# Performance work log

Measured on AMD Instinct MI355X. Metric: run time of the kernel, lower is better.

Reference implementation:

```python
import jax, jax.numpy as jnp
import numpy as np


def _rgcn_layer(h, Wr, Ws, src, dst, rel, norm):
    # h: [N,d], Wr: [R,d,d] per-relation weight, Ws: [d,d] self-loop weight
    N, d = h.shape
    R = Wr.shape[0]
    E = src.shape[0]
    msg = jnp.zeros((E, d), h.dtype)
    for r in range(R):  # R is small/static; transform-then-gather per relation
        hW = h @ Wr[r]              # [N,d]
        msg = jnp.where((rel == r)[:, None], hW[src], msg)  # [E,d]
    agg = jax.ops.segment_sum(msg * norm[:, None], dst, num_segments=N)
    return jax.nn.relu(agg + h @ Ws)


def _calc_score(emb, w_relation, es, er, eo):
    # DistMult-style bilinear score: s^T W_r o per target edge
    s = emb[es]                     # [T,d]
    o = emb[eo]                     # [T,d]
    R = w_relation.shape[0]
    sW = jnp.zeros_like(s)
    for r in range(R):
        sW = jnp.where((er == r)[:, None], s @ w_relation[r], sW)
    return jnp.sum(sW * o, axis=-1)  # [T]


def setup_inputs() -> dict:
    key = jax.random.key(0)
    ks = jax.random.split(key, 16)
    N, E, T, d, R, L = 20000, 160000, 50000, 768, 8, 2
    sc = 1.0 / np.sqrt(d)
    return {
        "node_feat": jax.random.normal(ks[0], (N, d), jnp.float32),
        "edge_norm": jax.random.uniform(ks[1], (E,), jnp.float32),
        "W_rel": jax.random.normal(ks[2], (L, R, d, d), jnp.float32) * sc,
        "W_self": jax.random.normal(ks[3], (L, d, d), jnp.float32) * sc,
        "w_relation": jax.random.normal(ks[4], (R, d, d), jnp.float32) * sc,
        "src": jax.random.randint(ks[5], (E,), 0, N, jnp.int32),
        "dst": jax.random.randint(ks[6], (E,), 0, N, jnp.int32),
        "rel": jax.random.randint(ks[7], (E,), 0, R, jnp.int32),
        "pos_src": jax.random.randint(ks[8], (T,), 0, N, jnp.int32),
        "pos_rel": jax.random.randint(ks[9], (T,), 0, R, jnp.int32),
        "pos_dst": jax.random.randint(ks[10], (T,), 0, N, jnp.int32),
        "neg_src": jax.random.randint(ks[11], (T,), 0, N, jnp.int32),
        "neg_rel": jax.random.randint(ks[12], (T,), 0, R, jnp.int32),
        "neg_dst": jax.random.randint(ks[13], (T,), 0, N, jnp.int32),
    }


def reference(node_feat, edge_norm, W_rel, W_self, w_relation,
              src, dst, rel, pos_src, pos_rel, pos_dst,
              neg_src, neg_rel, neg_dst):
    h = node_feat
    L = W_rel.shape[0]
    for l in range(L):
        h = _rgcn_layer(h, W_rel[l], W_self[l], src, dst, rel, edge_norm)
    es = jnp.concatenate([pos_src, neg_src])
    er = jnp.concatenate([pos_rel, neg_rel])
    eo = jnp.concatenate([pos_dst, neg_dst])
    score = _calc_score(h, w_relation, es, er, eo)  # [2T]
    return score
```

## Files before the change

### kernel.cpp

```cpp
#include <hip/hip_runtime.h>

typedef float f32x4 __attribute__((ext_vector_type(4)));
typedef __bf16 bf16x8 __attribute__((ext_vector_type(8)));
typedef unsigned short u16x8 __attribute__((ext_vector_type(8)));
typedef unsigned short u16x4 __attribute__((ext_vector_type(4)));

static __device__ __forceinline__ unsigned short f2bf(float f) {
  unsigned int x = __builtin_bit_cast(unsigned int, f);
  x += 0x7FFFu + ((x >> 16) & 1u);
  return (unsigned short)(x >> 16);
}
static __device__ __forceinline__ float bf2f(unsigned short h) {
  unsigned int x = ((unsigned int)h) << 16;
  return __builtin_bit_cast(float, x);
}

static __device__ __forceinline__ void gload_lds16(const unsigned short* g,
                                                   unsigned short* l) {
  __builtin_amdgcn_global_load_lds(
      (const __attribute__((address_space(1))) void*)g,
      (__attribute__((address_space(3))) void*)l, 16, 0, 0);
}

__global__ __launch_bounds__(256) void k_f32_to_bf16(
    const float* __restrict__ in, unsigned short* __restrict__ out, int n4) {
  int i = blockIdx.x * 256 + threadIdx.x;
  if (i >= n4) return;
  float4 v = reinterpret_cast<const float4*>(in)[i];
  u16x4 o = {f2bf(v.x), f2bf(v.y), f2bf(v.z), f2bf(v.w)};
  reinterpret_cast<u16x4*>(out)[i] = o;
}

__global__ __launch_bounds__(256) void k_transpose_w(
    const float* __restrict__ in, unsigned short* __restrict__ out,
    int G, int SL, int j0) {
  __shared__ float tile[32][33];
  const int D = 768;
  int z = blockIdx.z;
  int j = j0 + z % G, grp = z / G;
  const float* A = in + (size_t)z * D * D;
  const size_t ld = (size_t)SL * D;
  unsigned short* O = out + (size_t)grp * D * ld + (size_t)j * D;
  int nt = blockIdx.x * 32, kt = blockIdx.y * 32;
  int tx = threadIdx.x, ty = threadIdx.y;
#pragma unroll
  for (int i = 0; i < 4; ++i)
    tile[ty + i * 8][tx] = A[(size_t)(kt + ty + i * 8) * D + nt + tx];
  __syncthreads();
#pragma unroll
  for (int i = 0; i < 4; ++i)
    O[(size_t)(nt + ty + i * 8) * ld + kt + tx] = f2bf(tile[tx][ty + i * 8]);
}

__global__ __launch_bounds__(256) void k_hist(const int* __restrict__ dst,
                                              const int* __restrict__ rel,
                                              int* __restrict__ cnt, int E, int NV) {
  int e = blockIdx.x * 256 + threadIdx.x;
  if (e < E) atomicAdd(&cnt[rel[e] * NV + dst[e]], 1);
}

__global__ __launch_bounds__(256) void k_hist_t(
    const int* __restrict__ ps, const int* __restrict__ pr,
    const int* __restrict__ ns, const int* __restrict__ nr,
    int* __restrict__ cnt, int T, int NV) {
  int t = blockIdx.x * 256 + threadIdx.x;
  if (t >= 2 * T) return;
  int s = (t < T) ? ps[t] : ns[t - T];
  int r = (t < T) ? pr[t] : nr[t - T];
  atomicAdd(&cnt[r * NV + s], 1);
}

__global__ __launch_bounds__(256) void k_part(const int* __restrict__ cnt,
                                              int* __restrict__ bsum, int n) {
  __shared__ int wsums[4];
  int blk = blockIdx.x, tid = threadIdx.x;
  int base = blk * 1024 + tid * 4;
  int s = 0;
#pragma unroll
  for (int j = 0; j < 4; ++j) {
    int i = base + j;
    if (i < n) s += cnt[i];
  }
#pragma unroll
  for (int d = 1; d < 64; d <<= 1) s += __shfl_xor(s, d, 64);
  if ((tid & 63) == 0) wsums[tid >> 6] = s;
  __syncthreads();
  if (tid == 0) bsum[blk] = wsums[0] + wsums[1] + wsums[2] + wsums[3];
}

__global__ __launch_bounds__(1024) void k_scan_b(const int* __restrict__ bsum,
                                                 int* __restrict__ bscan, int nb,
                                                 int* __restrict__ off_total) {
  __shared__ int wpre[16];
  int tid = threadIdx.x, lane = tid & 63, w = tid >> 6;
  int v = (tid < nb) ? bsum[tid] : 0;
  int inc = v;
#pragma unroll
  for (int d = 1; d < 64; d <<= 1) {
    int t = __shfl_up(inc, d, 64);
    if (lane >= d) inc += t;
  }
  if (lane == 63) wpre[w] = inc;
  __syncthreads();
  if (w == 0) {
    int vv = (lane < 16) ? wpre[lane] : 0;
    int p = vv;
#pragma unroll
    for (int d = 1; d < 16; d <<= 1) {
      int t = __shfl_up(p, d, 64);
      if (lane >= d) p += t;
    }
    if (lane < 16) wpre[lane] = p - vv;
  }
  __syncthreads();
  if (tid < nb) bscan[tid] = wpre[w] + inc - v;
  if (tid == 1023) *off_total = wpre[15] + inc;
}

__global__ __launch_bounds__(256) void k_scan_f(const int* __restrict__ cnt,
                                                const int* __restrict__ bscan,
                                                int* __restrict__ off, int n) {
  __shared__ int wpre[4];
  int blk = blockIdx.x, tid = threadIdx.x, lane = tid & 63, w = tid >> 6;
  int base = blk * 1024 + tid * 4;
  int v[4];
  int s = 0;
#pragma unroll
  for (int j = 0; j < 4; ++j) {
    int i = base + j;
    v[j] = (i < n) ? cnt[i] : 0;
    s += v[j];
  }
  int inc = s;
#pragma unroll
  for (int d = 1; d < 64; d <<= 1) {
    int t = __shfl_up(inc, d, 64);
    if (lane >= d) inc += t;
  }
  if (lane == 63) wpre[w] = inc;
  __syncthreads();
  int wb = 0;
  for (int j = 0; j < w; ++j) wb += wpre[j];
  int run = bscan[blk] + wb + (inc - s);
#pragma unroll
  for (int j = 0; j < 4; ++j) {
    int i = base + j;
    if (i < n) off[i] = run;
    run += v[j];
  }
}

__global__ __launch_bounds__(256) void k_bucket(
    const int* __restrict__ src, const int* __restrict__ dst,
    const int* __restrict__ rel, const float* __restrict__ norm,
    const int* __restrict__ off, int* __restrict__ fill,
    int* __restrict__ spack, float* __restrict__ snorm, int E, int NV) {
  int e = blockIdx.x * 256 + threadIdx.x;
  if (e >= E) return;
  int key = rel[e] * NV + dst[e];
  int slot = off[key] + atomicAdd(&fill[key], 1);
  spack[slot] = src[e];
  snorm[slot] = norm[e];
}

__global__ __launch_bounds__(512) void k_tprep(
    const int* __restrict__ off2, int* __restrict__ tpo, int* __restrict__ rbase,
    int* __restrict__ btile, int NV, int R, int TB) {
  __shared__ int tpo_s[17];
  int tid = threadIdx.x;
  if (tid == 0) {
    int run = 0;
    for (int r = 0; r < R; ++r) {
      rbase[r] = off2[r * NV];
      int tot = off2[(r + 1) * NV] - off2[r * NV];
      tpo_s[r] = run;
      run += (tot + 255) & ~255;
    }
    tpo_s[R] = run;
    for (int r = 0; r <= R; ++r) tpo[r] = tpo_s[r];
  }
  __syncthreads();
  for (int mt = tid; mt < TB; mt += 512) {
    int base = mt * 256;
    int b = -1;
    if (base < tpo_s[R]) {
      for (int r = 0; r < R; ++r)
        if (base >= tpo_s[r] && base < tpo_s[r + 1]) { b = r; break; }
    }
    btile[mt] = b;
  }
}

__global__ __launch_bounds__(256) void k_tbucket3(
    const int* __restrict__ ps, const int* __restrict__ pr, const int* __restrict__ pd,
    const int* __restrict__ ns, const int* __restrict__ nr, const int* __restrict__ nd,
    const int* __restrict__ off2, int* __restrict__ fill,
    const int* __restrict__ tpo, const int* __restrict__ rbase,
    int* __restrict__ sidx, int* __restrict__ oidx, int* __restrict__ tmap,
    int T, int NV) {
  int t = blockIdx.x * 256 + threadIdx.x;
  if (t >= 2 * T) return;
  int s, r, o;
  if (t < T) { s = ps[t]; r = pr[t]; o = pd[t]; }
  else       { s = ns[t - T]; r = nr[t - T]; o = nd[t - T]; }
  int key = r * NV + s;
  int rank = atomicAdd(&fill[key], 1);
  int slot = tpo[r] + (off2[key] - rbase[r]) + rank;
  sidx[slot] = s;
  oidx[slot] = o;
  tmap[slot] = t;
}

__global__ __launch_bounds__(256) void k_gather(
    const unsigned short* __restrict__ h, const int* __restrict__ off,
    const int* __restrict__ spack, const float* __restrict__ snorm,
    unsigned short* __restrict__ Acat, int NV, int r0, int r1, int ld) {
  int v = (blockIdx.x * 256 + threadIdx.x) >> 6;
  int lane = threadIdx.x & 63;
  int col = lane * 4;
  for (int r = r0; r < r1; ++r) {
    float a[12];
#pragma unroll
    for (int j = 0; j < 12; ++j) a[j] = 0.f;
    if (v < NV) {
      int beg = off[r * NV + v], end = off[r * NV + v + 1];
      for (int p = beg; p < end; ++p) {
        const unsigned short* row = h + (size_t)spack[p] * 768 + col;
        float nm = snorm[p];
#pragma unroll
        for (int c = 0; c < 3; ++c) {
          u16x4 vv = *reinterpret_cast<const u16x4*>(row + c * 256);
#pragma unroll
          for (int j = 0; j < 4; ++j) a[c * 4 + j] += nm * bf2f(vv[j]);
        }
      }
    }
    unsigned short* orow = Acat + (size_t)v * ld + (size_t)(r - r0) * 768 + col;
#pragma unroll
    for (int c = 0; c < 3; ++c) {
      u16x4 o = {f2bf(a[c * 4 + 0]), f2bf(a[c * 4 + 1]),
                 f2bf(a[c * 4 + 2]), f2bf(a[c * 4 + 3])};
      *reinterpret_cast<u16x4*>(orow + c * 256) = o;
    }
  }
}

#define STAGE_A(BUF, HALF, TT)                                                   \
  do {                                                                           \
    const unsigned short* _s =                                                   \
        A + (size_t)(m0 + (HALF) * 128 + srow) * K + (size_t)(TT) * 64 + gcol;   \
    gload_lds16(_s, &As[BUF][HALF][w << 3][0]);                                  \
    gload_lds16(_s + (size_t)64 * K, &As[BUF][HALF][64 + (w << 3)][0]);          \
  } while (0)
#define STAGE_B(BUF, HALF, TT)                                                   \
  do {                                                                           \
    const unsigned short* _s =                                                   \
        B + (size_t)(n0 + (HALF) * 128 + srow) * K + (size_t)(TT) * 64 + gcol;   \
    gload_lds16(_s, &Bs[BUF][HALF][w << 3][0]);                                  \
    gload_lds16(_s + (size_t)64 * K, &Bs[BUF][HALF][64 + (w << 3)][0]);          \
  } while (0)
#define GEMM_PRE()                                                               \
  const int tid = threadIdx.x;                                                   \
  const int lane = tid & 63;                                                     \
  const int w = tid >> 6;                                                        \
  const int wr = w >> 2;                                                         \
  const int wc = w & 3;                                                          \
  const int lr = lane & 15, lg = lane >> 4;                                      \
  int bid = blockIdx.x;                                                          \
  const int per = 8 * NT;                                                        \
  int grp = bid / per, rem = bid % per;                                          \
  int mstart = grp * 8;                                                          \
  int gsz = MT - mstart;                                                         \
  if (gsz > 8) gsz = 8;                                                          \
  const int mt = mstart + rem % gsz;                                             \
  const int ntile = rem / gsz;                                                   \
  const int m0 = mt * 256, n0 = ntile * 256;                                     \
  const int srow = tid >> 3;                                                     \
  const int gcol = (((tid & 7) ^ (tid >> 3)) & 7) * 8;                           \
  const int nk = K >> 6;
#define R_BV6(BUF)                                                               \
  _Pragma("unroll") for (int nb = 0; nb < 2; ++nb)                               \
  _Pragma("unroll") for (int j = 0; j < 2; ++j)                                  \
  _Pragma("unroll") for (int kk = 0; kk < 2; ++kk)                               \
      bv[nb][j][kk] = *reinterpret_cast<const bf16x8*>(                          \
          &Bs[BUF][nb][wc * 32 + j * 16 + lr][((lg + 4 * kk) ^ (lr & 7)) * 8]);
#define R_AF6(BUF, HALF)                                                         \
  _Pragma("unroll") for (int i = 0; i < 4; ++i)                                  \
  _Pragma("unroll") for (int kk = 0; kk < 2; ++kk)                               \
      af[i][kk] = *reinterpret_cast<const bf16x8*>(                              \
          &As[BUF][HALF][wr * 64 + i * 16 + lr][((lg + 4 * kk) ^ (lr & 7)) * 8]);
#define GEMM_LOOP(STAGEA_MACRO)                                                  \
  bf16x8 af[4][2], bv[2][2][2];                                                  \
  for (int t = 0; t < nk; ++t) {                                                 \
    const int buf = t & 1;                                                       \
    if (t + 1 < nk)                                                              \
      asm volatile("s_waitcnt vmcnt(4)" ::: "memory");                           \
    else                                                                         \
      asm volatile("s_waitcnt vmcnt(0)" ::: "memory");                           \
    __builtin_amdgcn_s_barrier();                                                \
    asm volatile("" ::: "memory");                                               \
    R_AF6(buf, 0);                                                               \
    R_BV6(buf);                                                                  \
    if (t + 1 < nk) {                                                            \
      STAGEA_MACRO(buf ^ 1, 1, t + 1);                                           \
      STAGE_B(buf ^ 1, 0, t + 1);                                                \
    }                                                                            \
    __builtin_amdgcn_s_setprio(1);                                               \
    _Pragma("unroll") for (int i = 0; i < 4; ++i)                                \
    _Pragma("unroll") for (int nb = 0; nb < 2; ++nb)                             \
    _Pragma("unroll") for (int j = 0; j < 2; ++j)                                \
    _Pragma("unroll") for (int kk = 0; kk < 2; ++kk)                             \
        acc[0][nb][i][j] = __builtin_amdgcn_mfma_f32_16x16x32_bf16(              \
            af[i][kk], bv[nb][j][kk], acc[0][nb][i][j], 0, 0, 0);                \
    __builtin_amdgcn_s_setprio(0);                                               \
    asm volatile("" ::: "memory");                                               \
    __builtin_amdgcn_s_barrier();                                                \
    asm volatile("" ::: "memory");                                               \
    R_AF6(buf, 1);                                                               \
    if (t + 2 < nk) {                                                            \
      STAGEA_MACRO(buf, 0, t + 2);                                               \
      STAGE_B(buf, 1, t + 2);                                                    \
    }                                                                            \
    __builtin_amdgcn_s_setprio(1);                                               \
    _Pragma("unroll") for (int i = 0; i < 4; ++i)                                \
    _Pragma("unroll") for (int nb = 0; nb < 2; ++nb)                             \
    _Pragma("unroll") for (int j = 0; j < 2; ++j)                                \
    _Pragma("unroll") for (int kk = 0; kk < 2; ++kk)                             \
        acc[1][nb][i][j] = __builtin_amdgcn_mfma_f32_16x16x32_bf16(              \
            af[i][kk], bv[nb][j][kk], acc[1][nb][i][j], 0, 0, 0);                \
    __builtin_amdgcn_s_setprio(0);                                               \
  }

template <int EPI>
__global__ __launch_bounds__(512, 2) void k_gemm_tn(
    const unsigned short* __restrict__ A, const unsigned short* __restrict__ B,
    void* __restrict__ Cp, const float* __restrict__ C0,
    int M, int N, int K, int MT, int NT) {
  __shared__ unsigned short As[2][2][128][64];
  __shared__ unsigned short Bs[2][2][128][64];
  GEMM_PRE();
  f32x4 acc[2][2][4][2] = {};

  STAGE_A(0, 0, 0);
  STAGE_B(0, 1, 0);
  STAGE_A(0, 1, 0);
  STAGE_B(0, 0, 0);
  if (nk > 1) {
    STAGE_A(1, 0, 1);
    STAGE_B(1, 1, 1);
  }
  GEMM_LOOP(STAGE_A);

#pragma unroll
  for (int ma = 0; ma < 2; ++ma)
#pragma unroll
    for (int i = 0; i < 4; ++i)
#pragma unroll
      for (int q = 0; q < 4; ++q) {
        int r = m0 + ma * 128 + wr * 64 + i * 16 + lg * 4 + q;
        if (r >= M) continue;
#pragma unroll
        for (int nb = 0; nb < 2; ++nb)
#pragma unroll
          for (int j = 0; j < 2; ++j) {
            int cn = n0 + nb * 128 + wc * 32 + j * 16 + lr;
            float v = acc[ma][nb][i][j][q];
            size_t idx = (size_t)r * N + cn;
            if (EPI == 1) {
              v += C0[idx];
              v = v > 0.f ? v : 0.f;
              ((unsigned short*)Cp)[idx] = f2bf(v);
            } else {
              ((float*)Cp)[idx] = v + C0[idx];
            }
          }
      }
}

#define STAGE_AH(BUF, HALF, TT)                                                  \
  do {                                                                           \
    const unsigned short* _sa =                                                  \
        ((TT) < nkA) ? paA##HALF##a + (size_t)(TT) * 64                          \
                     : paH##HALF##a + (size_t)((TT)-nkA) * 64;                   \
    gload_lds16(_sa, &As[BUF][HALF][w << 3][0]);                                 \
    const unsigned short* _sb =                                                  \
        ((TT) < nkA) ? paA##HALF##b + (size_t)(TT) * 64                          \
                     : paH##HALF##b + (size_t)((TT)-nkA) * 64;                   \
    gload_lds16(_sb, &As[BUF][HALF][64 + (w << 3)][0]);                          \
  } while (0)

__global__ __launch_bounds__(512, 2) void k_gemm_fuse(
    const unsigned short* __restrict__ Ac, const unsigned short* __restrict__ hA,
    const unsigned short* __restrict__ B, float* __restrict__ Cp,
    int M, int N, int K, int KA, int MT, int NT) {
  __shared__ unsigned short As[2][2][128][64];
  __shared__ unsigned short Bs[2][2][128][64];
  GEMM_PRE();
  const int nkA = KA >> 6;
  const unsigned short* paA0a = Ac + (size_t)(m0 + srow) * KA + gcol;
  const unsigned short* paA0b = Ac + (size_t)(m0 + 64 + srow) * KA + gcol;
  const unsigned short* paA1a = Ac + (size_t)(m0 + 128 + srow) * KA + gcol;
  const unsigned short* paA1b = Ac + (size_t)(m0 + 192 + srow) * KA + gcol;
  const unsigned short* paH0a = hA + (size_t)(m0 + srow) * 768 + gcol;
  const unsigned short* paH0b = hA + (size_t)(m0 + 64 + srow) * 768 + gcol;
  const unsigned short* paH1a = hA + (size_t)(m0 + 128 + srow) * 768 + gcol;
  const unsigned short* paH1b = hA + (size_t)(m0 + 192 + srow) * 768 + gcol;

  f32x4 acc[2][2][4][2] = {};

  STAGE_AH(0, 0, 0);
  STAGE_B(0, 1, 0);
  STAGE_AH(0, 1, 0);
  STAGE_B(0, 0, 0);
  if (nk > 1) {
    STAGE_AH(1, 0, 1);
    STAGE_B(1, 1, 1);
  }
  GEMM_LOOP(STAGE_AH);

#pragma unroll
  for (int ma = 0; ma < 2; ++ma)
#pragma unroll
    for (int i = 0; i < 4; ++i)
#pragma unroll
      for (int q = 0; q < 4; ++q) {
        int r = m0 + ma * 128 + wr * 64 + i * 16 + lg * 4 + q;
        if (r >= M) continue;
#pragma unroll
        for (int nb = 0; nb < 2; ++nb)
#pragma unroll
          for (int j = 0; j < 2; ++j) {
            int cn = n0 + nb * 128 + wc * 32 + j * 16 + lr;
            Cp[(size_t)r * N + cn] = acc[ma][nb][i][j][q];
          }
      }
}

#define STAGE_AI(BUF, HALF, TT)                                                  \
  do {                                                                           \
    gload_lds16(pa##HALF##a + (size_t)(TT) * 64, &As[BUF][HALF][w << 3][0]);     \
    gload_lds16(pa##HALF##b + (size_t)(TT) * 64,                                 \
                &As[BUF][HALF][64 + (w << 3)][0]);                               \
  } while (0)

__global__ __launch_bounds__(512, 2) void k_gemm_score(
    const unsigned short* __restrict__ h, const unsigned short* __restrict__ Bw,
    float* __restrict__ out, const int* __restrict__ sidx,
    const int* __restrict__ oidx, const int* __restrict__ tmap,
    const int* __restrict__ btile, int MT, int NT) {
  const int K = 768;
  __shared__ unsigned short As[2][2][128][64];
  __shared__ unsigned short Bs[2][2][128][64];
  GEMM_PRE();
  const int bt = btile[mt];
  if (bt < 0) return;
  const unsigned short* B = Bw + (size_t)bt * K * K;
  const unsigned short* pa0a = h + (size_t)sidx[m0 + srow] * K + gcol;
  const unsigned short* pa0b = h + (size_t)sidx[m0 + 64 + srow] * K + gcol;
  const unsigned short* pa1a = h + (size_t)sidx[m0 + 128 + srow] * K + gcol;
  const unsigned short* pa1b = h + (size_t)sidx[m0 + 192 + srow] * K + gcol;

  f32x4 acc[2][2][4][2] = {};

  STAGE_AI(0, 0, 0);
  STAGE_B(0, 1, 0);
  STAGE_AI(0, 1, 0);
  STAGE_B(0, 0, 0);
  STAGE_AI(1, 0, 1);
  STAGE_B(1, 1, 1);
  GEMM_LOOP(STAGE_AI);

#pragma unroll
  for (int ma = 0; ma < 2; ++ma)
#pragma unroll
    for (int i = 0; i < 4; ++i)
#pragma unroll
      for (int q = 0; q < 4; ++q) {
        int slot = m0 + ma * 128 + wr * 64 + i * 16 + lg * 4 + q;
        int t = tmap[slot];
        float p = 0.f;
        if (t >= 0) {
          const unsigned short* orow = h + (size_t)oidx[slot] * K;
#pragma unroll
          for (int nb = 0; nb < 2; ++nb)
#pragma unroll
            for (int j = 0; j < 2; ++j) {
              int cn = n0 + nb * 128 + wc * 32 + j * 16 + lr;
              p += acc[ma][nb][i][j][q] * bf2f(orow[cn]);
            }
        }
#pragma unroll
        for (int d = 1; d < 16; d <<= 1) p += __shfl_xor(p, d, 64);
        if (t >= 0 && lr == 0) unsafeAtomicAdd(&out[t], p);
      }
}

extern "C" void kernel_launch(void* const* d_in, const int* in_sizes, int n_in,
                              void* d_out, int out_size, void* d_ws, size_t ws_size,
                              hipStream_t stream) {
  const float* node_feat = (const float*)d_in[0];
  const float* edge_norm = (const float*)d_in[1];
  const float* W_rel = (const float*)d_in[2];
  const float* W_self = (const float*)d_in[3];
  const float* w_relation = (const float*)d_in[4];
  const int* src = (const int*)d_in[5];
  const int* dst = (const int*)d_in[6];
  const int* rel = (const int*)d_in[7];
  const int* pos_src = (const int*)d_in[8];
  const int* pos_rel = (const int*)d_in[9];
  const int* pos_dst = (const int*)d_in[10];
  const int* neg_src = (const int*)d_in[11];
  const int* neg_rel = (const int*)d_in[12];
  const int* neg_dst = (const int*)d_in[13];

  const int D = 768;
  const int NV = in_sizes[0] / D;
  const int E = in_sizes[1];
  const int L = in_sizes[3] / (D * D);
  const int R = in_sizes[4] / (D * D);
  const int T = in_sizes[8];
  const int Mpad = (NV + 255) & ~255;
  const int RN = R * NV;
  const int NB = (RN + 1023) / 1024;
  const int TB = (2 * T + R * 256 + 255) / 256;
  const int Mbound = TB * 256;

  auto align_up = [](size_t x) { return (x + 255) & ~(size_t)255; };
  size_t sz_wt_rel = align_up((size_t)L * (R + 1) * D * D * 2);
  size_t sz_wt_score = align_up((size_t)R * D * D * 2);
  size_t sz_h = align_up((size_t)Mpad * D * 2);
  size_t sz_agg = align_up((size_t)Mpad * D * 4);
  size_t sz_cntfill = align_up((size_t)2 * RN * 4);
  size_t sz_off = align_up((size_t)(RN + 8) * 4);
  size_t sz_sp = align_up((size_t)E * 4);
  size_t sz_bs = align_up((size_t)2 * (NB + 8) * 4);
  size_t sz_tix = align_up((size_t)Mbound * 4);
  size_t sz_tsmall = align_up((size_t)(TB + 64) * 4);
  size_t fixed = sz_wt_rel + sz_wt_score + sz_h + sz_agg + sz_cntfill +
                 2 * sz_off + 2 * sz_sp + sz_bs + 3 * sz_tix + sz_tsmall;
  int RG = 4;
  while (RG > 1 && fixed + align_up((size_t)Mpad * RG * D * 2) > ws_size) RG >>= 1;
  const int NGRP = R / RG;
  const size_t LW = (size_t)(R + 1) * D * D;

  char* wp = (char*)d_ws;
  unsigned short* wt_rel = (unsigned short*)wp; wp += sz_wt_rel;
  unsigned short* wt_score = (unsigned short*)wp; wp += sz_wt_score;
  unsigned short* h = (unsigned short*)wp; wp += sz_h;
  float* agg = (float*)wp; wp += sz_agg;
  int* cnt = (int*)wp; int* fill = cnt + RN; wp += sz_cntfill;
  int* off = (int*)wp; wp += sz_off;
  int* off2 = (int*)wp; wp += sz_off;
  int* spack = (int*)wp; wp += sz_sp;
  float* snorm = (float*)wp; wp += sz_sp;
  int* bsum = (int*)wp; int* bscan = bsum + NB + 4; wp += sz_bs;
  int* sidx = (int*)wp; wp += sz_tix;
  int* oidx = (int*)wp; wp += sz_tix;
  int* tmap = (int*)wp; wp += sz_tix;
  int* btile = (int*)wp;
  int* tpo = btile + TB + 8;
  int* rbase = tpo + R + 2;
  wp += sz_tsmall;
  unsigned short* Acat = (unsigned short*)wp;

  dim3 tb32(32, 8);
  k_f32_to_bf16<<<(NV * D / 4 + 255) / 256, 256, 0, stream>>>(node_feat, h, NV * D / 4);
  if (Mpad > NV)
    hipMemsetAsync(h + (size_t)NV * D, 0, (size_t)(Mpad - NV) * D * 2, stream);
  for (int l = 0; l < L; ++l) {
    k_transpose_w<<<dim3(24, 24, RG), tb32, 0, stream>>>(
        W_rel + (size_t)l * R * D * D, wt_rel + (size_t)l * LW, RG, RG + 1, 0);
    k_transpose_w<<<dim3(24, 24, 1), tb32, 0, stream>>>(
        W_self + (size_t)l * D * D, wt_rel + (size_t)l * LW, 1, RG + 1, RG);
    for (int gi = 1; gi < NGRP; ++gi)
      k_transpose_w<<<dim3(24, 24, RG), tb32, 0, stream>>>(
          W_rel + (size_t)(l * R + gi * RG) * D * D,
          wt_rel + (size_t)l * LW + (size_t)(RG + 1) * D * D +
              (size_t)(gi - 1) * RG * D * D, RG, RG, 0);
  }
  k_transpose_w<<<dim3(24, 24, R), tb32, 0, stream>>>(w_relation, wt_score, 1, 1, 0);

  hipMemsetAsync(cnt, 0, (size_t)2 * RN * 4, stream);
  k_hist<<<(E + 255) / 256, 256, 0, stream>>>(dst, rel, cnt, E, NV);
  k_part<<<NB, 256, 0, stream>>>(cnt, bsum, RN);
  k_scan_b<<<1, 1024, 0, stream>>>(bsum, bscan, NB, off + RN);
  k_scan_f<<<NB, 256, 0, stream>>>(cnt, bscan, off, RN);
  k_bucket<<<(E + 255) / 256, 256, 0, stream>>>(src, dst, rel, edge_norm, off, fill,
                                                spack, snorm, E, NV);

  hipMemsetAsync(cnt, 0, (size_t)2 * RN * 4, stream);
  k_hist_t<<<(2 * T + 255) / 256, 256, 0, stream>>>(pos_src, pos_rel,
                                                    neg_src, neg_rel, cnt, T, NV);
  k_part<<<NB, 256, 0, stream>>>(cnt, bsum, RN);
  k_scan_b<<<1, 1024, 0, stream>>>(bsum, bscan, NB, off2 + RN);
  k_scan_f<<<NB, 256, 0, stream>>>(cnt, bscan, off2, RN);
  k_tprep<<<1, 512, 0, stream>>>(off2, tpo, rbase, btile, NV, R, TB);
  hipMemsetAsync(sidx, 0, sz_tix, stream);
  hipMemsetAsync(tmap, 0xFF, sz_tix, stream);
  hipMemsetAsync(d_out, 0, (size_t)2 * T * 4, stream);
  k_tbucket3<<<(2 * T + 255) / 256, 256, 0, stream>>>(
      pos_src, pos_rel, pos_dst, neg_src, neg_rel, neg_dst,
      off2, fill, tpo, rbase, sidx, oidx, tmap, T, NV);

  const int MT = Mpad / 256;
  const int KG = RG * D;
  const int gblocks = Mpad / 4;
  for (int l = 0; l < L; ++l) {
    k_gather<<<gblocks, 256, 0, stream>>>(h, off, spack, snorm, Acat, NV, 0, RG, KG);
    k_gemm_fuse<<<MT * 3, 512, 0, stream>>>(
        Acat, h, wt_rel + (size_t)l * LW, agg, NV, D, KG + D, KG, MT, 3);
    for (int gi = 1; gi < NGRP; ++gi) {
      k_gather<<<gblocks, 256, 0, stream>>>(h, off, spack, snorm, Acat, NV,
                                            gi * RG, gi * RG + RG, KG);
      const unsigned short* Bw = wt_rel + (size_t)l * LW +
                                 (size_t)(RG + 1) * D * D +
                                 (size_t)(gi - 1) * RG * D * D;
      if (gi == NGRP - 1)
        k_gemm_tn<1><<<MT * 3, 512, 0, stream>>>(Acat, Bw, h, agg, NV, D, KG, MT, 3);
      else
        k_gemm_tn<3><<<MT * 3, 512, 0, stream>>>(Acat, Bw, agg, agg, NV, D, KG, MT, 3);
    }
  }
  k_gemm_score<<<TB * 3, 512, 0, stream>>>(h, wt_score, (float*)d_out,
                                           sidx, oidx, tmap, btile, TB, 3);
}
```

Baseline: 873.6 us.

## Add 128x128-tile GEMM kernels for scoring and first-layer relation GEMMs

Adds a simpler 256-thread GEMM family with 128x128 output tiles and a K-step of 32, using a single LDS buffer with XOR swizzling. It replaces the 256-tile score GEMM and, for layer 0 only, the fused and grouped relation GEMMs. The smaller tiles reduce per-relation padding in the scoring buckets and give more blocks for occupancy. In exchange they drop the double-buffered, waitcnt-pipelined loads and add two barriers per K-step, which exposes memory latency. The layer-0-only switch looks like an A/B comparison against the old kernels.

```diff
diff --git a/kernel.cpp b/kernel.cpp
--- a/kernel.cpp
+++ b/kernel.cpp
@@ -165,7 +165,7 @@
 
 __global__ __launch_bounds__(512) void k_tprep(
     const int* __restrict__ off2, int* __restrict__ tpo, int* __restrict__ rbase,
-    int* __restrict__ btile, int NV, int R, int TB) {
+    int* __restrict__ btile, int NV, int R, int TB, int TILE) {
   __shared__ int tpo_s[17];
   int tid = threadIdx.x;
   if (tid == 0) {
@@ -174,14 +174,14 @@
       rbase[r] = off2[r * NV];
       int tot = off2[(r + 1) * NV] - off2[r * NV];
       tpo_s[r] = run;
-      run += (tot + 255) & ~255;
+      run += (tot + TILE - 1) & ~(TILE - 1);
     }
     tpo_s[R] = run;
     for (int r = 0; r <= R; ++r) tpo[r] = tpo_s[r];
   }
   __syncthreads();
   for (int mt = tid; mt < TB; mt += 512) {
-    int base = mt * 256;
+    int base = mt * TILE;
     int b = -1;
     if (base < tpo_s[R]) {
       for (int r = 0; r < R; ++r)
@@ -259,12 +259,10 @@
     gload_lds16(_s, &Bs[BUF][HALF][w << 3][0]);                                  \
     gload_lds16(_s + (size_t)64 * K, &Bs[BUF][HALF][64 + (w << 3)][0]);          \
   } while (0)
-#define GEMM_PRE()                                                               \
+#define GEMM_PRE(TSZ)                                                            \
   const int tid = threadIdx.x;                                                   \
   const int lane = tid & 63;                                                     \
   const int w = tid >> 6;                                                        \
-  const int wr = w >> 2;                                                         \
-  const int wc = w & 3;                                                          \
   const int lr = lane & 15, lg = lane >> 4;                                      \
   int bid = blockIdx.x;                                                          \
   const int per = 8 * NT;                                                        \
@@ -274,10 +272,7 @@
   if (gsz > 8) gsz = 8;                                                          \
   const int mt = mstart + rem % gsz;                                             \
   const int ntile = rem / gsz;                                                   \
-  const int m0 = mt * 256, n0 = ntile * 256;                                     \
-  const int srow = tid >> 3;                                                     \
-  const int gcol = (((tid & 7) ^ (tid >> 3)) & 7) * 8;                           \
-  const int nk = K >> 6;
+  const int m0 = mt * (TSZ), n0 = ntile * (TSZ);
 #define R_BV6(BUF)                                                               \
   _Pragma("unroll") for (int nb = 0; nb < 2; ++nb)                               \
   _Pragma("unroll") for (int j = 0; j < 2; ++j)                                  \
@@ -338,7 +333,11 @@
     int M, int N, int K, int MT, int NT) {
   __shared__ unsigned short As[2][2][128][64];
   __shared__ unsigned short Bs[2][2][128][64];
-  GEMM_PRE();
+  GEMM_PRE(256);
+  const int wr = w >> 2, wc = w & 3;
+  const int srow = tid >> 3;
+  const int gcol = (((tid & 7) ^ (tid >> 3)) & 7) * 8;
+  const int nk = K >> 6;
   f32x4 acc[2][2][4][2] = {};
 
   STAGE_A(0, 0, 0);
@@ -395,7 +394,11 @@
     int M, int N, int K, int KA, int MT, int NT) {
   __shared__ unsigned short As[2][2][128][64];
   __shared__ unsigned short Bs[2][2][128][64];
-  GEMM_PRE();
+  GEMM_PRE(256);
+  const int wr = w >> 2, wc = w & 3;
+  const int srow = tid >> 3;
+  const int gcol = (((tid & 7) ^ (tid >> 3)) & 7) * 8;
+  const int nk = K >> 6;
   const int nkA = KA >> 6;
   const unsigned short* paA0a = Ac + (size_t)(m0 + srow) * KA + gcol;
   const unsigned short* paA0b = Ac + (size_t)(m0 + 64 + srow) * KA + gcol;
@@ -436,63 +439,149 @@
       }
 }
 
-#define STAGE_AI(BUF, HALF, TT)                                                  \
-  do {                                                                           \
-    gload_lds16(pa##HALF##a + (size_t)(TT) * 64, &As[BUF][HALF][w << 3][0]);     \
-    gload_lds16(pa##HALF##b + (size_t)(TT) * 64,                                 \
-                &As[BUF][HALF][64 + (w << 3)][0]);                               \
-  } while (0)
-
-__global__ __launch_bounds__(512, 2) void k_gemm_score(
+#define G128_PRE()                                                               \
+  const int wr = w >> 1, wc = w & 1;                                             \
+  const int srow = w * 32 + (lane >> 2);                                         \
+  const int cs = lane & 3;                                                       \
+  const int gc0 = (cs ^ ((srow >> 1) & 3)) * 8;                                  \
+  const int gc1 = (cs ^ (((srow + 16) >> 1) & 3)) * 8;                           \
+  unsigned short* la = a_lds + w * 1024;                                         \
+  unsigned short* lb = b_lds + w * 1024;                                         \
+  const int ro = (lg ^ ((lr >> 1) & 3)) * 8;
+#define G128_STEP(PA0, PA1, PB0, PB1)                                            \
+  __syncthreads();                                                               \
+  gload_lds16(PA0, la);                                                          \
+  gload_lds16(PA1, la + 512);                                                    \
+  gload_lds16(PB0, lb);                                                          \
+  gload_lds16(PB1, lb + 512);                                                    \
+  __syncthreads();                                                               \
+  {                                                                              \
+    bf16x8 af[4], bfv[4];                                                        \
+    _Pragma("unroll") for (int i = 0; i < 4; ++i)                                \
+        af[i] = *reinterpret_cast<const bf16x8*>(                                \
+            a_lds + (wr * 64 + i * 16 + lr) * 32 + ro);                          \
+    _Pragma("unroll") for (int j = 0; j < 4; ++j)                                \
+        bfv[j] = *reinterpret_cast<const bf16x8*>(                               \
+            b_lds + (wc * 64 + j * 16 + lr) * 32 + ro);                          \
+    _Pragma("unroll") for (int i = 0; i < 4; ++i)                                \
+        _Pragma("unroll") for (int j = 0; j < 4; ++j)                            \
+            acc[i][j] = __builtin_amdgcn_mfma_f32_16x16x32_bf16(                 \
+                af[i], bfv[j], acc[i][j], 0, 0, 0);                              \
+  }
+
+template <int EPI>
+__global__ __launch_bounds__(256) void k_gemm_tn128(
+    const unsigned short* __restrict__ A, const unsigned short* __restrict__ B,
+    void* __restrict__ Cp, const float* __restrict__ C0,
+    int M, int N, int K, int MT, int NT) {
+  __shared__ unsigned short a_lds[128 * 32];
+  __shared__ unsigned short b_lds[128 * 32];
+  GEMM_PRE(128);
+  G128_PRE();
+  const unsigned short* pa0 = A + (size_t)(m0 + srow) * K + gc0;
+  const unsigned short* pa1 = A + (size_t)(m0 + srow + 16) * K + gc1;
+  const unsigned short* pb0 = B + (size_t)(n0 + srow) * K + gc0;
+  const unsigned short* pb1 = B + (size_t)(n0 + srow + 16) * K + gc1;
+  f32x4 acc[4][4] = {};
+  for (int k0 = 0; k0 < K; k0 += 32) {
+    G128_STEP(pa0 + k0, pa1 + k0, pb0 + k0, pb1 + k0);
+  }
+#pragma unroll
+  for (int i = 0; i < 4; ++i)
+#pragma unroll
+    for (int q = 0; q < 4; ++q) {
+      int r = m0 + wr * 64 + i * 16 + lg * 4 + q;
+      if (r >= M) continue;
+#pragma unroll
+      for (int j = 0; j < 4; ++j) {
+        int cn = n0 + wc * 64 + j * 16 + lr;
+        float v = acc[i][j][q];
+        size_t idx = (size_t)r * N + cn;
+        if (EPI == 1) {
+          v += C0[idx];
+          v = v > 0.f ? v : 0.f;
+          ((unsigned short*)Cp)[idx] = f2bf(v);
+        } else {
+          ((float*)Cp)[idx] = v + C0[idx];
+        }
+      }
+    }
+}
+
+__global__ __launch_bounds__(256) void k_gemm_fuse128(
+    const unsigned short* __restrict__ Ac, const unsigned short* __restrict__ hA,
+    const unsigned short* __restrict__ B, float* __restrict__ Cp,
+    int M, int N, int K, int KA, int MT, int NT) {
+  __shared__ unsigned short a_lds[128 * 32];
+  __shared__ unsigned short b_lds[128 * 32];
+  GEMM_PRE(128);
+  G128_PRE();
+  const unsigned short* paA0 = Ac + (size_t)(m0 + srow) * KA + gc0;
+  const unsigned short* paA1 = Ac + (size_t)(m0 + srow + 16) * KA + gc1;
+  const unsigned short* paH0 = hA + (size_t)(m0 + srow) * 768 + gc0;
+  const unsigned short* paH1 = hA + (size_t)(m0 + srow + 16) * 768 + gc1;
+  const unsigned short* pb0 = B + (size_t)(n0 + srow) * K + gc0;
+  const unsigned short* pb1 = B + (size_t)(n0 + srow + 16) * K + gc1;
+  f32x4 acc[4][4] = {};
+  for (int k0 = 0; k0 < K; k0 += 32) {
+    const unsigned short* s0 = (k0 < KA) ? paA0 + k0 : paH0 + (k0 - KA);
+    const unsigned short* s1 = (k0 < KA) ? paA1 + k0 : paH1 + (k0 - KA);
+    G128_STEP(s0, s1, pb0 + k0, pb1 + k0);
+  }
+#pragma unroll
+  for (int i = 0; i < 4; ++i)
+#pragma unroll
+    for (int q = 0; q < 4; ++q) {
+      int r = m0 + wr * 64 + i * 16 + lg * 4 + q;
+      if (r >= M) continue;
+#pragma unroll
+      for (int j = 0; j < 4; ++j) {
+        int cn = n0 + wc * 64 + j * 16 + lr;
+        Cp[(size_t)r * N + cn] = acc[i][j][q];
+      }
+    }
+}
+
+__global__ __launch_bounds__(256) void k_gemm_score128(
     const unsigned short* __restrict__ h, const unsigned short* __restrict__ Bw,
     float* __restrict__ out, const int* __restrict__ sidx,
     const int* __restrict__ oidx, const int* __restrict__ tmap,
     const int* __restrict__ btile, int MT, int NT) {
   const int K = 768;
-  __shared__ unsigned short As[2][2][128][64];
-  __shared__ unsigned short Bs[2][2][128][64];
-  GEMM_PRE();
+  __shared__ unsigned short a_lds[128 * 32];
+  __shared__ unsigned short b_lds[128 * 32];
+  GEMM_PRE(128);
   const int bt = btile[mt];
   if (bt < 0) return;
+  G128_PRE();
   const unsigned short* B = Bw + (size_t)bt * K * K;
-  const unsigned short* pa0a = h + (size_t)sidx[m0 + srow] * K + gcol;
-  const unsigned short* pa0b = h + (size_t)sidx[m0 + 64 + srow] * K + gcol;
-  const unsigned short* pa1a = h + (size_t)sidx[m0 + 128 + srow] * K + gcol;
-  const unsigned short* pa1b = h + (size_t)sidx[m0 + 192 + srow] * K + gcol;
-
-  f32x4 acc[2][2][4][2] = {};
-
-  STAGE_AI(0, 0, 0);
-  STAGE_B(0, 1, 0);
-  STAGE_AI(0, 1, 0);
-  STAGE_B(0, 0, 0);
-  STAGE_AI(1, 0, 1);
-  STAGE_B(1, 1, 1);
-  GEMM_LOOP(STAGE_AI);
-
-#pragma unroll
-  for (int ma = 0; ma < 2; ++ma)
-#pragma unroll
-    for (int i = 0; i < 4; ++i)
-#pragma unroll
-      for (int q = 0; q < 4; ++q) {
-        int slot = m0 + ma * 128 + wr * 64 + i * 16 + lg * 4 + q;
-        int t = tmap[slot];
-        float p = 0.f;
-        if (t >= 0) {
-          const unsigned short* orow = h + (size_t)oidx[slot] * K;
-#pragma unroll
-          for (int nb = 0; nb < 2; ++nb)
-#pragma unroll
-            for (int j = 0; j < 2; ++j) {
-              int cn = n0 + nb * 128 + wc * 32 + j * 16 + lr;
-              p += acc[ma][nb][i][j][q] * bf2f(orow[cn]);
-            }
+  const unsigned short* pa0 = h + (size_t)sidx[m0 + srow] * K + gc0;
+  const unsigned short* pa1 = h + (size_t)sidx[m0 + srow + 16] * K + gc1;
+  const unsigned short* pb0 = B + (size_t)(n0 + srow) * K + gc0;
+  const unsigned short* pb1 = B + (size_t)(n0 + srow + 16) * K + gc1;
+  f32x4 acc[4][4] = {};
+  for (int k0 = 0; k0 < K; k0 += 32) {
+    G128_STEP(pa0 + k0, pa1 + k0, pb0 + k0, pb1 + k0);
+  }
+#pragma unroll
+  for (int i = 0; i < 4; ++i)
+#pragma unroll
+    for (int q = 0; q < 4; ++q) {
+      int slot = m0 + wr * 64 + i * 16 + lg * 4 + q;
+      int t = tmap[slot];
+      float p = 0.f;
+      if (t >= 0) {
+        const unsigned short* orow = h + (size_t)oidx[slot] * K;
+#pragma unroll
+        for (int j = 0; j < 4; ++j) {
+          int cn = n0 + wc * 64 + j * 16 + lr;
+          p += acc[i][j][q] * bf2f(orow[cn]);
         }
-#pragma unroll
-        for (int d = 1; d < 16; d <<= 1) p += __shfl_xor(p, d, 64);
-        if (t >= 0 && lr == 0) unsafeAtomicAdd(&out[t], p);
       }
+#pragma unroll
+      for (int d = 1; d < 16; d <<= 1) p += __shfl_xor(p, d, 64);
+      if (t >= 0 && lr == 0) unsafeAtomicAdd(&out[t], p);
+    }
 }
 
 extern "C" void kernel_launch(void* const* d_in, const int* in_sizes, int n_in,
@@ -522,8 +611,8 @@
   const int Mpad = (NV + 255) & ~255;
   const int RN = R * NV;
   const int NB = (RN + 1023) / 1024;
-  const int TB = (2 * T + R * 256 + 255) / 256;
-  const int Mbound = TB * 256;
+  const int TB = (2 * T + R * 128 + 127) / 128;
+  const int Mbound = TB * 128;
 
   auto align_up = [](size_t x) { return (x + 255) & ~(size_t)255; };
   size_t sz_wt_rel = align_up((size_t)L * (R + 1) * D * D * 2);
@@ -594,7 +683,7 @@
   k_part<<<NB, 256, 0, stream>>>(cnt, bsum, RN);
   k_scan_b<<<1, 1024, 0, stream>>>(bsum, bscan, NB, off2 + RN);
   k_scan_f<<<NB, 256, 0, stream>>>(cnt, bscan, off2, RN);
-  k_tprep<<<1, 512, 0, stream>>>(off2, tpo, rbase, btile, NV, R, TB);
+  k_tprep<<<1, 512, 0, stream>>>(off2, tpo, rbase, btile, NV, R, TB, 128);
   hipMemsetAsync(sidx, 0, sz_tix, stream);
   hipMemsetAsync(tmap, 0xFF, sz_tix, stream);
   hipMemsetAsync(d_out, 0, (size_t)2 * T * 4, stream);
@@ -603,24 +692,40 @@
       off2, fill, tpo, rbase, sidx, oidx, tmap, T, NV);
 
   const int MT = Mpad / 256;
+  const int MT128 = Mpad / 128;
   const int KG = RG * D;
   const int gblocks = Mpad / 4;
   for (int l = 0; l < L; ++l) {
     k_gather<<<gblocks, 256, 0, stream>>>(h, off, spack, snorm, Acat, NV, 0, RG, KG);
-    k_gemm_fuse<<<MT * 3, 512, 0, stream>>>(
-        Acat, h, wt_rel + (size_t)l * LW, agg, NV, D, KG + D, KG, MT, 3);
+    if (l == 0)
+      k_gemm_fuse128<<<MT128 * 6, 256, 0, stream>>>(
+          Acat, h, wt_rel + (size_t)l * LW, agg, NV, D, KG + D, KG, MT128, 6);
+    else
+      k_gemm_fuse<<<MT * 3, 512, 0, stream>>>(
+          Acat, h, wt_rel + (size_t)l * LW, agg, NV, D, KG + D, KG, MT, 3);
     for (int gi = 1; gi < NGRP; ++gi) {
       k_gather<<<gblocks, 256, 0, stream>>>(h, off, spack, snorm, Acat, NV,
                                             gi * RG, gi * RG + RG, KG);
       const unsigned short* Bw = wt_rel + (size_t)l * LW +
                                  (size_t)(RG + 1) * D * D +
                                  (size_t)(gi - 1) * RG * D * D;
-      if (gi == NGRP - 1)
-        k_gemm_tn<1><<<MT * 3, 512, 0, stream>>>(Acat, Bw, h, agg, NV, D, KG, MT, 3);
-      else
-        k_gemm_tn<3><<<MT * 3, 512, 0, stream>>>(Acat, Bw, agg, agg, NV, D, KG, MT, 3);
-    }
-  }
-  k_gemm_score<<<TB * 3, 512, 0, stream>>>(h, wt_score, (float*)d_out,
-                                           sidx, oidx, tmap, btile, TB, 3);
-}
+      if (gi == NGRP - 1) {
+        if (l == 0)
+          k_gemm_tn128<1><<<MT128 * 6, 256, 0, stream>>>(Acat, Bw, h, agg, NV, D,
+                                                         KG, MT128, 6);
+        else
+          k_gemm_tn<1><<<MT * 3, 512, 0, stream>>>(Acat, Bw, h, agg, NV, D, KG,
+                                                   MT, 3);
+      } else {
+        if (l == 0)
+          k_gemm_tn128<3><<<MT128 * 6, 256, 0, stream>>>(Acat, Bw, agg, agg, NV, D,
+                                                         KG, MT128, 6);
+        else
+          k_gemm_tn<3><<<MT * 3, 512, 0, stream>>>(Acat, Bw, agg, agg, NV, D, KG,
+                                                   MT, 3);
+      }
+    }
+  }
+  k_gemm_score128<<<TB * 6, 256, 0, stream>>>(h, wt_score, (float*)d_out,
+                                              sidx, oidx, tmap, btile, TB, 6);
+}
```

Result: slower. 1.006 ms (+15.1%).

## Deduplicate (subject, relation) rows in score GEMM and fan out to objects

Applied to the files above, without the earlier changes.

Scoring triples are now grouped by unique (relation, subject) key. An extra indicator scan compacts the keys, so the score GEMM computes each s·W_r row only once, and its epilogue loops over every object that shares that key. This cuts redundant GEMM rows when triples repeat a subject-relation pair. In exchange it adds several small scan and prep kernels, plus a variable-length epilogue loop with more atomics per row.

```diff
diff --git a/kernel.cpp b/kernel.cpp
--- a/kernel.cpp
+++ b/kernel.cpp
@@ -70,6 +70,12 @@
   atomicAdd(&cnt[r * NV + s], 1);
 }
 
+__global__ __launch_bounds__(256) void k_ind(const int* __restrict__ cnt,
+                                             int* __restrict__ ind, int n) {
+  int i = blockIdx.x * 256 + threadIdx.x;
+  if (i < n) ind[i] = cnt[i] ? 1 : 0;
+}
+
 __global__ __launch_bounds__(256) void k_part(const int* __restrict__ cnt,
                                               int* __restrict__ bsum, int n) {
   __shared__ int wsums[4];
@@ -163,16 +169,16 @@
   snorm[slot] = norm[e];
 }
 
-__global__ __launch_bounds__(512) void k_tprep(
-    const int* __restrict__ off2, int* __restrict__ tpo, int* __restrict__ rbase,
+__global__ __launch_bounds__(512) void k_tprep_u(
+    const int* __restrict__ uoff, int* __restrict__ tpo, int* __restrict__ urbase,
     int* __restrict__ btile, int NV, int R, int TB) {
   __shared__ int tpo_s[17];
   int tid = threadIdx.x;
   if (tid == 0) {
     int run = 0;
     for (int r = 0; r < R; ++r) {
-      rbase[r] = off2[r * NV];
-      int tot = off2[(r + 1) * NV] - off2[r * NV];
+      urbase[r] = uoff[r * NV];
+      int tot = uoff[(r + 1) * NV] - uoff[r * NV];
       tpo_s[r] = run;
       run += (tot + 255) & ~255;
     }
@@ -191,24 +197,34 @@
   }
 }
 
-__global__ __launch_bounds__(256) void k_tbucket3(
+__global__ __launch_bounds__(256) void k_uprep(
+    const int* __restrict__ cnt, const int* __restrict__ uoff,
+    const int* __restrict__ off2, const int* __restrict__ tpo,
+    const int* __restrict__ urbase, int* __restrict__ sidx,
+    int* __restrict__ dbeg, int* __restrict__ dcnt, int RN, int NV) {
+  int key = blockIdx.x * 256 + threadIdx.x;
+  if (key >= RN || cnt[key] == 0) return;
+  int r = key / NV;
+  int slot = tpo[r] + (uoff[key] - urbase[r]);
+  sidx[slot] = key - r * NV;
+  dbeg[slot] = off2[key];
+  dcnt[slot] = cnt[key];
+}
+
+__global__ __launch_bounds__(256) void k_tbucket_t(
     const int* __restrict__ ps, const int* __restrict__ pr, const int* __restrict__ pd,
     const int* __restrict__ ns, const int* __restrict__ nr, const int* __restrict__ nd,
     const int* __restrict__ off2, int* __restrict__ fill,
-    const int* __restrict__ tpo, const int* __restrict__ rbase,
-    int* __restrict__ sidx, int* __restrict__ oidx, int* __restrict__ tmap,
-    int T, int NV) {
+    int* __restrict__ oidx2, int* __restrict__ tmap2, int T, int NV) {
   int t = blockIdx.x * 256 + threadIdx.x;
   if (t >= 2 * T) return;
   int s, r, o;
   if (t < T) { s = ps[t]; r = pr[t]; o = pd[t]; }
   else       { s = ns[t - T]; r = nr[t - T]; o = nd[t - T]; }
   int key = r * NV + s;
-  int rank = atomicAdd(&fill[key], 1);
-  int slot = tpo[r] + (off2[key] - rbase[r]) + rank;
-  sidx[slot] = s;
-  oidx[slot] = o;
-  tmap[slot] = t;
+  int pos = off2[key] + atomicAdd(&fill[key], 1);
+  oidx2[pos] = o;
+  tmap2[pos] = t;
 }
 
 __global__ __launch_bounds__(256) void k_gather(
@@ -446,7 +462,8 @@
 __global__ __launch_bounds__(512, 2) void k_gemm_score(
     const unsigned short* __restrict__ h, const unsigned short* __restrict__ Bw,
     float* __restrict__ out, const int* __restrict__ sidx,
-    const int* __restrict__ oidx, const int* __restrict__ tmap,
+    const int* __restrict__ dbeg, const int* __restrict__ dcnt,
+    const int* __restrict__ oidx2, const int* __restrict__ tmap2,
     const int* __restrict__ btile, int MT, int NT) {
   const int K = 768;
   __shared__ unsigned short As[2][2][128][64];
@@ -477,21 +494,22 @@
 #pragma unroll
       for (int q = 0; q < 4; ++q) {
         int slot = m0 + ma * 128 + wr * 64 + i * 16 + lg * 4 + q;
-        int t = tmap[slot];
-        float p = 0.f;
-        if (t >= 0) {
-          const unsigned short* orow = h + (size_t)oidx[slot] * K;
+        int dc = dcnt[slot];
+        int db = dbeg[slot];
+        for (int p = 0; p < dc; ++p) {
+          const unsigned short* orow = h + (size_t)oidx2[db + p] * K;
+          float pp = 0.f;
 #pragma unroll
           for (int nb = 0; nb < 2; ++nb)
 #pragma unroll
             for (int j = 0; j < 2; ++j) {
               int cn = n0 + nb * 128 + wc * 32 + j * 16 + lr;
-              p += acc[ma][nb][i][j][q] * bf2f(orow[cn]);
+              pp += acc[ma][nb][i][j][q] * bf2f(orow[cn]);
             }
+#pragma unroll
+          for (int d2 = 1; d2 < 16; d2 <<= 1) pp += __shfl_xor(pp, d2, 64);
+          if (lr == 0) unsafeAtomicAdd(&out[tmap2[db + p]], pp);
         }
-#pragma unroll
-        for (int d = 1; d < 16; d <<= 1) p += __shfl_xor(p, d, 64);
-        if (t >= 0 && lr == 0) unsafeAtomicAdd(&out[t], p);
       }
 }
 
@@ -535,9 +553,11 @@
   size_t sz_sp = align_up((size_t)E * 4);
   size_t sz_bs = align_up((size_t)2 * (NB + 8) * 4);
   size_t sz_tix = align_up((size_t)Mbound * 4);
+  size_t sz_t2 = align_up((size_t)(2 * T + 8) * 4);
   size_t sz_tsmall = align_up((size_t)(TB + 64) * 4);
   size_t fixed = sz_wt_rel + sz_wt_score + sz_h + sz_agg + sz_cntfill +
-                 2 * sz_off + 2 * sz_sp + sz_bs + 3 * sz_tix + sz_tsmall;
+                 4 * sz_off + 2 * sz_sp + sz_bs + 3 * sz_tix + 2 * sz_t2 +
+                 sz_tsmall;
   int RG = 4;
   while (RG > 1 && fixed + align_up((size_t)Mpad * RG * D * 2) > ws_size) RG >>= 1;
   const int NGRP = R / RG;
@@ -551,15 +571,19 @@
   int* cnt = (int*)wp; int* fill = cnt + RN; wp += sz_cntfill;
   int* off = (int*)wp; wp += sz_off;
   int* off2 = (int*)wp; wp += sz_off;
+  int* ind = (int*)wp; wp += sz_off;
+  int* uoff = (int*)wp; wp += sz_off;
   int* spack = (int*)wp; wp += sz_sp;
   float* snorm = (float*)wp; wp += sz_sp;
   int* bsum = (int*)wp; int* bscan = bsum + NB + 4; wp += sz_bs;
   int* sidx = (int*)wp; wp += sz_tix;
-  int* oidx = (int*)wp; wp += sz_tix;
-  int* tmap = (int*)wp; wp += sz_tix;
+  int* dbeg = (int*)wp; wp += sz_tix;
+  int* dcnt = (int*)wp; wp += sz_tix;
+  int* oidx2 = (int*)wp; wp += sz_t2;
+  int* tmap2 = (int*)wp; wp += sz_t2;
   int* btile = (int*)wp;
   int* tpo = btile + TB + 8;
-  int* rbase = tpo + R + 2;
+  int* urbase = tpo + R + 2;
   wp += sz_tsmall;
   unsigned short* Acat = (unsigned short*)wp;
 
@@ -594,13 +618,19 @@
   k_part<<<NB, 256, 0, stream>>>(cnt, bsum, RN);
   k_scan_b<<<1, 1024, 0, stream>>>(bsum, bscan, NB, off2 + RN);
   k_scan_f<<<NB, 256, 0, stream>>>(cnt, bscan, off2, RN);
-  k_tprep<<<1, 512, 0, stream>>>(off2, tpo, rbase, btile, NV, R, TB);
+  k_ind<<<(RN + 255) / 256, 256, 0, stream>>>(cnt, ind, RN);
+  k_part<<<NB, 256, 0, stream>>>(ind, bsum, RN);
+  k_scan_b<<<1, 1024, 0, stream>>>(bsum, bscan, NB, uoff + RN);
+  k_scan_f<<<NB, 256, 0, stream>>>(ind, bscan, uoff, RN);
+  k_tprep_u<<<1, 512, 0, stream>>>(uoff, tpo, urbase, btile, NV, R, TB);
   hipMemsetAsync(sidx, 0, sz_tix, stream);
-  hipMemsetAsync(tmap, 0xFF, sz_tix, stream);
+  hipMemsetAsync(dcnt, 0, sz_tix, stream);
   hipMemsetAsync(d_out, 0, (size_t)2 * T * 4, stream);
-  k_tbucket3<<<(2 * T + 255) / 256, 256, 0, stream>>>(
+  k_uprep<<<(RN + 255) / 256, 256, 0, stream>>>(cnt, uoff, off2, tpo, urbase,
+                                                sidx, dbeg, dcnt, RN, NV);
+  k_tbucket_t<<<(2 * T + 255) / 256, 256, 0, stream>>>(
       pos_src, pos_rel, pos_dst, neg_src, neg_rel, neg_dst,
-      off2, fill, tpo, rbase, sidx, oidx, tmap, T, NV);
+      off2, fill, oidx2, tmap2, T, NV);
 
   const int MT = Mpad / 256;
   const int KG = RG * D;
@@ -622,5 +652,6 @@
     }
   }
   k_gemm_score<<<TB * 3, 512, 0, stream>>>(h, wt_score, (float*)d_out,
-                                           sidx, oidx, tmap, btile, TB, 3);
-}
+                                           sidx, dbeg, dcnt, oidx2, tmap2,
+                                           btile, TB, 3);
+}
```

After: 1.031 ms. 18.0% more time.

## Process all relations in one fused GEMM with ReLU+bf16 epilogue and ping-pong h

Applied to the files above, without the earlier changes.

The relation-group size now starts at all R relations instead of 4, so when workspace allows, each layer runs one gather and one fused GEMM. That GEMM applies ReLU and writes bf16 directly into a second h buffer. This removes the fp32 aggregation buffer round trips and the extra gather/GEMM launches per group. In exchange, the concatenated A buffer becomes much larger (Mpad*R*D bf16), and the path depends on workspace size. The old multi-group path is kept as a fallback.

```diff
diff --git a/kernel.cpp b/kernel.cpp
--- a/kernel.cpp
+++ b/kernel.cpp
@@ -389,9 +389,10 @@
     gload_lds16(_sb, &As[BUF][HALF][64 + (w << 3)][0]);                          \
   } while (0)
 
+template <int EPI>
 __global__ __launch_bounds__(512, 2) void k_gemm_fuse(
     const unsigned short* __restrict__ Ac, const unsigned short* __restrict__ hA,
-    const unsigned short* __restrict__ B, float* __restrict__ Cp,
+    const unsigned short* __restrict__ B, void* __restrict__ Cp,
     int M, int N, int K, int KA, int MT, int NT) {
   __shared__ unsigned short As[2][2][128][64];
   __shared__ unsigned short Bs[2][2][128][64];
@@ -431,7 +432,14 @@
 #pragma unroll
           for (int j = 0; j < 2; ++j) {
             int cn = n0 + nb * 128 + wc * 32 + j * 16 + lr;
-            Cp[(size_t)r * N + cn] = acc[ma][nb][i][j][q];
+            float v = acc[ma][nb][i][j][q];
+            size_t idx = (size_t)r * N + cn;
+            if (EPI == 2) {
+              ((float*)Cp)[idx] = v;
+            } else {
+              v = v > 0.f ? v : 0.f;
+              ((unsigned short*)Cp)[idx] = f2bf(v);
+            }
           }
       }
 }
@@ -536,10 +544,15 @@
   size_t sz_bs = align_up((size_t)2 * (NB + 8) * 4);
   size_t sz_tix = align_up((size_t)Mbound * 4);
   size_t sz_tsmall = align_up((size_t)(TB + 64) * 4);
-  size_t fixed = sz_wt_rel + sz_wt_score + sz_h + sz_agg + sz_cntfill +
+  size_t fixed = sz_wt_rel + sz_wt_score + 2 * sz_h + sz_cntfill +
                  2 * sz_off + 2 * sz_sp + sz_bs + 3 * sz_tix + sz_tsmall;
-  int RG = 4;
-  while (RG > 1 && fixed + align_up((size_t)Mpad * RG * D * 2) > ws_size) RG >>= 1;
+  int RG = R;
+  while (RG > 1) {
+    size_t need = fixed + ((RG < R) ? sz_agg : 0) +
+                  align_up((size_t)Mpad * RG * D * 2);
+    if (need <= ws_size) break;
+    RG >>= 1;
+  }
   const int NGRP = R / RG;
   const size_t LW = (size_t)(R + 1) * D * D;
 
@@ -547,7 +560,7 @@
   unsigned short* wt_rel = (unsigned short*)wp; wp += sz_wt_rel;
   unsigned short* wt_score = (unsigned short*)wp; wp += sz_wt_score;
   unsigned short* h = (unsigned short*)wp; wp += sz_h;
-  float* agg = (float*)wp; wp += sz_agg;
+  unsigned short* h2 = (unsigned short*)wp; wp += sz_h;
   int* cnt = (int*)wp; int* fill = cnt + RN; wp += sz_cntfill;
   int* off = (int*)wp; wp += sz_off;
   int* off2 = (int*)wp; wp += sz_off;
@@ -561,6 +574,8 @@
   int* tpo = btile + TB + 8;
   int* rbase = tpo + R + 2;
   wp += sz_tsmall;
+  float* agg = nullptr;
+  if (NGRP > 1) { agg = (float*)wp; wp += sz_agg; }
   unsigned short* Acat = (unsigned short*)wp;
 
   dim3 tb32(32, 8);
@@ -605,22 +620,35 @@
   const int MT = Mpad / 256;
   const int KG = RG * D;
   const int gblocks = Mpad / 4;
+  unsigned short* hcur = h;
+  unsigned short* hnext = h2;
   for (int l = 0; l < L; ++l) {
-    k_gather<<<gblocks, 256, 0, stream>>>(h, off, spack, snorm, Acat, NV, 0, RG, KG);
-    k_gemm_fuse<<<MT * 3, 512, 0, stream>>>(
-        Acat, h, wt_rel + (size_t)l * LW, agg, NV, D, KG + D, KG, MT, 3);
-    for (int gi = 1; gi < NGRP; ++gi) {
-      k_gather<<<gblocks, 256, 0, stream>>>(h, off, spack, snorm, Acat, NV,
-                                            gi * RG, gi * RG + RG, KG);
-      const unsigned short* Bw = wt_rel + (size_t)l * LW +
-                                 (size_t)(RG + 1) * D * D +
-                                 (size_t)(gi - 1) * RG * D * D;
-      if (gi == NGRP - 1)
-        k_gemm_tn<1><<<MT * 3, 512, 0, stream>>>(Acat, Bw, h, agg, NV, D, KG, MT, 3);
-      else
-        k_gemm_tn<3><<<MT * 3, 512, 0, stream>>>(Acat, Bw, agg, agg, NV, D, KG, MT, 3);
+    if (NGRP == 1) {
+      k_gather<<<gblocks, 256, 0, stream>>>(hcur, off, spack, snorm, Acat, NV,
+                                            0, R, KG);
+      k_gemm_fuse<4><<<MT * 3, 512, 0, stream>>>(
+          Acat, hcur, wt_rel + (size_t)l * LW, hnext, NV, D, KG + D, KG, MT, 3);
+      unsigned short* tmp = hcur; hcur = hnext; hnext = tmp;
+    } else {
+      k_gather<<<gblocks, 256, 0, stream>>>(hcur, off, spack, snorm, Acat, NV,
+                                            0, RG, KG);
+      k_gemm_fuse<2><<<MT * 3, 512, 0, stream>>>(
+          Acat, hcur, wt_rel + (size_t)l * LW, agg, NV, D, KG + D, KG, MT, 3);
+      for (int gi = 1; gi < NGRP; ++gi) {
+        k_gather<<<gblocks, 256, 0, stream>>>(hcur, off, spack, snorm, Acat, NV,
+                                              gi * RG, gi * RG + RG, KG);
+        const unsigned short* Bw = wt_rel + (size_t)l * LW +
+                                   (size_t)(RG + 1) * D * D +
+                                   (size_t)(gi - 1) * RG * D * D;
+        if (gi == NGRP - 1)
+          k_gemm_tn<1><<<MT * 3, 512, 0, stream>>>(Acat, Bw, hcur, agg, NV, D, KG,
+                                                   MT, 3);
+        else
+          k_gemm_tn<3><<<MT * 3, 512, 0, stream>>>(Acat, Bw, agg, agg, NV, D, KG,
+                                                   MT, 3);
+      }
     }
   }
-  k_gemm_score<<<TB * 3, 512, 0, stream>>>(h, wt_score, (float*)d_out,
+  k_gemm_score<<<TB * 3, 512, 0, stream>>>(hcur, wt_score, (float*)d_out,
                                            sidx, oidx, tmap, btile, TB, 3);
 }
```

After: 966.6 us. 1.11x slower.
